# Kernel tuning notes

Measured on AMD Instinct MI355X. Metric: run time of the kernel, lower is better.

The kernel has to match this reference:

```python
import jax, jax.numpy as jnp
import numpy as np

NW = 30000      # num_words (word nodes)
ND = 8192       # num_docs
D = 300         # hidden_dim
D2 = D // 2
NNZ_A = 600000  # nnz of word-word adjacency A_norm [NW, NW]
NNZ_X = 524288  # nnz of doc-word tfidf X [ND, NW]
ALPHA = 0.7     # residual_alpha
LN_EPS = 1e-5
BN_SCALE = float(1.0 / np.sqrt(1.0 + 1e-5))  # eval BN, running_mean=0, running_var=1


def _xavier(k, shape):
    fan_out, fan_in = shape[0], shape[1]
    lim = float(np.sqrt(6.0 / (fan_in + fan_out)))
    return jax.random.uniform(k, shape, jnp.float32, -lim, lim)


def setup_inputs() -> dict:
    key = jax.random.key(0)
    ks = jax.random.split(key, 13)
    return {
        "a_rows": jax.random.randint(ks[0], (NNZ_A,), 0, NW, dtype=jnp.int32),
        "a_cols": jax.random.randint(ks[1], (NNZ_A,), 0, NW, dtype=jnp.int32),
        "a_vals": jax.random.uniform(ks[2], (NNZ_A,), jnp.float32) * 0.05,
        "x_rows": jax.random.randint(ks[3], (NNZ_X,), 0, ND, dtype=jnp.int32),
        "x_cols": jax.random.randint(ks[4], (NNZ_X,), 0, NW, dtype=jnp.int32),
        "x_vals": jax.random.uniform(ks[5], (NNZ_X,), jnp.float32) * 0.05,
        "emb": _xavier(ks[6], (NW, D)),
        "w1": _xavier(ks[7], (D, D)),
        "w2": _xavier(ks[8], (D, D)),
        "w3": _xavier(ks[9], (D, D)),
        "ln_g": jnp.ones((D,), jnp.float32),
        "ln_b": jnp.zeros((D,), jnp.float32),
        "m_w1": _xavier(ks[10], (D, D)),
        "m_b1": jnp.zeros((D,), jnp.float32),
        "bn1_g": jnp.ones((D,), jnp.float32),
        "bn1_b": jnp.zeros((D,), jnp.float32),
        "m_w2": _xavier(ks[11], (D2, D)),
        "m_b2": jnp.zeros((D2,), jnp.float32),
        "bn2_g": jnp.ones((D2,), jnp.float32),
        "bn2_b": jnp.zeros((D2,), jnp.float32),
        "clf_w": _xavier(ks[12], (2, D2)),
        "clf_b": jnp.zeros((2,), jnp.float32),
    }


def _spmm(rows, cols, vals, H, n):
    # sparse [n, m] @ dense [m, d] via gather + segment-sum (COO SpMM)
    return jax.ops.segment_sum(vals[:, None] * H[cols], rows, num_segments=n)


def _layernorm(x, g, b):
    mu = jnp.mean(x, axis=-1, keepdims=True)
    var = jnp.var(x, axis=-1, keepdims=True)
    return (x - mu) * jax.lax.rsqrt(var + LN_EPS) * g + b


def _bn_eval(x, g, b):
    # BatchNorm1d in eval mode with freshly-initialized running stats (mean=0, var=1)
    return x * (g * BN_SCALE) + b


def reference(a_rows, a_cols, a_vals, x_rows, x_cols, x_vals, emb, w1, w2, w3,
              ln_g, ln_b, m_w1, m_b1, bn1_g, bn1_b, m_w2, m_b2, bn2_g, bn2_b,
              clf_w, clf_b):
    H0 = emb
    H = jax.nn.relu(_spmm(a_rows, a_cols, a_vals, H0, NW) @ w1.T)
    H = jax.nn.relu(_spmm(a_rows, a_cols, a_vals, H, NW) @ w2.T)
    H = jax.nn.relu(_spmm(a_rows, a_cols, a_vals, H, NW) @ w3.T)
    H = (1.0 - ALPHA) * H0 + ALPHA * H
    word_H = _layernorm(H, ln_g, ln_b)
    # --- doc aggregation: X_tfidf @ word_H + X_tfidf @ emb ---
    doc_H = (_spmm(x_rows, x_cols, x_vals, word_H, ND)
             + _spmm(x_rows, x_cols, x_vals, emb, ND))
    # --- MLP head (dropout inactive in eval) ---
    h = jax.nn.relu(_bn_eval(doc_H @ m_w1.T + m_b1, bn1_g, bn1_b))
    h = jax.nn.relu(_bn_eval(h @ m_w2.T + m_b2, bn2_g, bn2_b))
    return h @ clf_w.T + clf_b  # [ND, 2]
```

## Files before the change

### kernel.cpp

```cpp
#include <hip/hip_runtime.h>

#define NW 30000
#define ND 8192
#define DIM 300
#define DIM2 150
#define NNZA 600000
#define NNZX 524288
#define PD 320
#define PD_U 160
#define BN_SCALE 0.99999500003749971f

typedef unsigned int uint;
typedef unsigned short ushort;
typedef __attribute__((ext_vector_type(8))) short bf16x8;
typedef __attribute__((ext_vector_type(4))) float f32x4;
typedef __attribute__((ext_vector_type(4))) uint uint4v;

static inline int cdiv(int a, int b){ return (a + b - 1) / b; }

__device__ __forceinline__ float b2f_lo(uint u){ return __builtin_bit_cast(float, u << 16); }
__device__ __forceinline__ float b2f_hi(uint u){ return __builtin_bit_cast(float, u & 0xffff0000u); }
__device__ __forceinline__ ushort f2b(float f){
  uint u = __builtin_bit_cast(uint, f);
  u += 0x7fffu + ((u >> 16) & 1u);
  return (ushort)(u >> 16);
}
__device__ __forceinline__ uint packb(float x, float y){
  return (uint)f2b(x) | ((uint)f2b(y) << 16);
}

__global__ void k_hist(const int* __restrict__ rows, int n, int* __restrict__ cnt){
  int i = blockIdx.x * blockDim.x + threadIdx.x;
  if (i < n) atomicAdd(&cnt[rows[i]], 1);
}

__global__ void k_copy_int(const int* __restrict__ a, int* __restrict__ b, int n){
  int i = blockIdx.x * blockDim.x + threadIdx.x;
  if (i < n) b[i] = a[i];
}

__global__ __launch_bounds__(1024) void k_bsum(const int* __restrict__ cnt, int n, int* __restrict__ bs){
  __shared__ int sd[1024];
  int t = threadIdx.x;
  int i = blockIdx.x * 1024 + t;
  sd[t] = (i < n) ? cnt[i] : 0;
  __syncthreads();
  #pragma unroll
  for (int o = 512; o > 0; o >>= 1){
    if (t < o) sd[t] += sd[t + o];
    __syncthreads();
  }
  if (t == 0) bs[blockIdx.x] = sd[0];
}

__global__ __launch_bounds__(64) void k_scan_small(int* __restrict__ bs, int nb,
                                                   int* __restrict__ rp, int n){
  int t = threadIdx.x;
  int orig = (t < nb) ? bs[t] : 0;
  int v = orig;
  #pragma unroll
  for (int o = 1; o < 64; o <<= 1){
    int x = __shfl_up(v, o);
    if (t >= o) v += x;
  }
  if (t < nb) bs[t] = v - orig;
  if (t == nb - 1) rp[n] = v;
}

__global__ __launch_bounds__(1024) void k_scan_apply(const int* __restrict__ cnt, int n,
        const int* __restrict__ bs, int* __restrict__ rp){
  __shared__ int sd[1024];
  int t = threadIdx.x;
  int i = blockIdx.x * 1024 + t;
  int v = (i < n) ? cnt[i] : 0;
  sd[t] = v;
  __syncthreads();
  for (int o = 1; o < 1024; o <<= 1){
    int x = (t >= o) ? sd[t - o] : 0;
    __syncthreads();
    sd[t] += x;
    __syncthreads();
  }
  if (i < n) rp[i] = bs[blockIdx.x] + sd[t] - v;
}

__global__ void k_scatter(const int* __restrict__ rows, const int* __restrict__ cols,
                          const float* __restrict__ vals, int n, int* __restrict__ cursor,
                          int* __restrict__ cs, float* __restrict__ vs){
  int i = blockIdx.x * blockDim.x + threadIdx.x;
  if (i < n){
    int r = rows[i];
    int p = atomicAdd(&cursor[r], 1);
    cs[p] = cols[i];
    vs[p] = vals[i];
  }
}

__global__ void k_f2b_pad8(const float* __restrict__ src, ushort* __restrict__ dst,
                           int srows, int scols, int drows, int dstride){
  int q = blockIdx.x * blockDim.x + threadIdx.x;
  int perRow = dstride >> 3;
  int r = q / perRow;
  int c = (q - r * perRow) << 3;
  if (r >= drows) return;
  float x[8];
  #pragma unroll
  for (int j = 0; j < 8; ++j)
    x[j] = (r < srows && c + j < scols) ? src[(size_t)r * scols + c + j] : 0.f;
  uint4v o;
  o.x = packb(x[0], x[1]); o.y = packb(x[2], x[3]);
  o.z = packb(x[4], x[5]); o.w = packb(x[6], x[7]);
  *(uint4v*)(dst + (size_t)r * dstride + c) = o;
}

__global__ __launch_bounds__(256) void k_spmm_b(const int* __restrict__ rp, const int* __restrict__ cs,
        const float* __restrict__ vs, const uint* __restrict__ Hb, uint* __restrict__ Ob, int nrows){
  int wid = (blockIdx.x * blockDim.x + threadIdx.x) >> 6;
  int lane = threadIdx.x & 63;
  if (wid >= nrows) return;
  int s = rp[wid], e = rp[wid + 1];
  const bool half = lane < 32;
  float acc[4][6] = {};
  int k = s;
  for (; k + 4 <= e; k += 4){
    #pragma unroll
    for (int j = 0; j < 4; ++j){
      int c = cs[k + j];
      float v = vs[k + j];
      const uint* p = Hb + (size_t)c * PD_U;
      uint u0 = p[lane], u1 = p[lane + 64];
      uint u2 = half ? p[lane + 128] : 0;
      acc[j][0] = fmaf(v, b2f_lo(u0), acc[j][0]);
      acc[j][1] = fmaf(v, b2f_hi(u0), acc[j][1]);
      acc[j][2] = fmaf(v, b2f_lo(u1), acc[j][2]);
      acc[j][3] = fmaf(v, b2f_hi(u1), acc[j][3]);
      acc[j][4] = fmaf(v, b2f_lo(u2), acc[j][4]);
      acc[j][5] = fmaf(v, b2f_hi(u2), acc[j][5]);
    }
  }
  for (; k < e; ++k){
    int c = cs[k];
    float v = vs[k];
    const uint* p = Hb + (size_t)c * PD_U;
    uint u0 = p[lane], u1 = p[lane + 64];
    uint u2 = half ? p[lane + 128] : 0;
    acc[0][0] = fmaf(v, b2f_lo(u0), acc[0][0]);
    acc[0][1] = fmaf(v, b2f_hi(u0), acc[0][1]);
    acc[0][2] = fmaf(v, b2f_lo(u1), acc[0][2]);
    acc[0][3] = fmaf(v, b2f_hi(u1), acc[0][3]);
    acc[0][4] = fmaf(v, b2f_lo(u2), acc[0][4]);
    acc[0][5] = fmaf(v, b2f_hi(u2), acc[0][5]);
  }
  #pragma unroll
  for (int d = 0; d < 6; ++d)
    acc[0][d] += (acc[1][d] + acc[2][d]) + acc[3][d];
  uint* o = Ob + (size_t)wid * PD_U;
  o[lane] = packb(acc[0][0], acc[0][1]);
  o[lane + 64] = packb(acc[0][2], acc[0][3]);
  if (half) o[lane + 128] = packb(acc[0][4], acc[0][5]);
}

__global__ __launch_bounds__(256) void k_mgemm(const ushort* __restrict__ A, const ushort* __restrict__ B,
        const float* __restrict__ bias, const float* __restrict__ bng, const float* __restrict__ bnb,
        ushort* __restrict__ C, int M, int Nvalid, int ldc, int relu){
  __shared__ ushort As[128][72];
  __shared__ ushort Bs[160][72];
  const int t = threadIdx.x;
  const int wid = t >> 6, lane = t & 63;
  const int bm = blockIdx.y << 7;
  const int bn = blockIdx.x * 160;
  const int wm = (wid >> 1) << 6;
  const int wn = (wid & 1) * 80;
  const int r16 = lane & 15;
  const int h8 = (lane >> 4) << 3;
  f32x4 acc[4][5] = {};
  for (int k0 = 0; k0 < PD; k0 += 64){
    #pragma unroll
    for (int i = 0; i < 4; ++i){
      int q = t + (i << 8);
      int r = q >> 3, c = (q & 7) << 3;
      int gm = bm + r; if (gm >= M) gm = M - 1;
      *(bf16x8*)(&As[r][c]) = *(const bf16x8*)(A + (size_t)gm * PD + k0 + c);
    }
    #pragma unroll
    for (int i = 0; i < 5; ++i){
      int q = t + (i << 8);
      int r = q >> 3, c = (q & 7) << 3;
      *(bf16x8*)(&Bs[r][c]) = *(const bf16x8*)(B + (size_t)(bn + r) * PD + k0 + c);
    }
    __syncthreads();
    #pragma unroll
    for (int kk = 0; kk < 2; ++kk){
      bf16x8 af[4], bfr[5];
      #pragma unroll
      for (int m = 0; m < 4; ++m)
        af[m] = *(const bf16x8*)(&As[wm + m * 16 + r16][kk * 32 + h8]);
      #pragma unroll
      for (int n = 0; n < 5; ++n)
        bfr[n] = *(const bf16x8*)(&Bs[wn + n * 16 + r16][kk * 32 + h8]);
      #pragma unroll
      for (int m = 0; m < 4; ++m)
        #pragma unroll
        for (int n = 0; n < 5; ++n)
          acc[m][n] = __builtin_amdgcn_mfma_f32_16x16x32_bf16(af[m], bfr[n], acc[m][n], 0, 0, 0);
    }
    __syncthreads();
  }
  const int cr = (lane >> 4) << 2;
  #pragma unroll
  for (int m = 0; m < 4; ++m){
    #pragma unroll
    for (int n = 0; n < 5; ++n){
      int col = bn + wn + n * 16 + r16;
      #pragma unroll
      for (int j = 0; j < 4; ++j){
        int row = bm + wm + m * 16 + cr + j;
        if (row >= M) continue;
        float v = acc[m][n][j];
        if (col < Nvalid){
          if (bias) v += bias[col];
          if (bng)  v = v * (bng[col] * BN_SCALE) + bnb[col];
          if (relu) v = fmaxf(v, 0.f);
        } else v = 0.f;
        C[(size_t)row * ldc + col] = f2b(v);
      }
    }
  }
}

__global__ __launch_bounds__(64) void k_res_ln(const float* __restrict__ emb, const uint* __restrict__ Hb,
        const float* __restrict__ g, const float* __restrict__ bb, uint* __restrict__ S){
  int row = blockIdx.x, lane = threadIdx.x;
  const float* e = emb + (size_t)row * DIM;
  const uint* h = Hb + (size_t)row * PD_U;
  float x[6], ev[6];
  float sum = 0.f, sq = 0.f;
  #pragma unroll
  for (int j = 0; j < 3; ++j){
    int i = lane + j * 64;
    float e0 = 0.f, e1 = 0.f, h0 = 0.f, h1 = 0.f;
    if (i < 150){
      uint u = h[i];
      h0 = b2f_lo(u); h1 = b2f_hi(u);
      e0 = e[2 * i]; e1 = e[2 * i + 1];
    }
    float v0 = 0.3f * e0 + 0.7f * h0;
    float v1 = 0.3f * e1 + 0.7f * h1;
    if (i >= 150){ v0 = 0.f; v1 = 0.f; }
    x[2*j] = v0; x[2*j+1] = v1; ev[2*j] = e0; ev[2*j+1] = e1;
    sum += v0 + v1; sq += v0 * v0 + v1 * v1;
  }
  #pragma unroll
  for (int o = 32; o > 0; o >>= 1){ sum += __shfl_down(sum, o); sq += __shfl_down(sq, o); }
  sum = __shfl(sum, 0); sq = __shfl(sq, 0);
  const float inv = 1.f / (float)DIM;
  float mu = sum * inv;
  float var = sq * inv - mu * mu;
  float rs = rsqrtf(var + 1e-5f);
  uint* o = S + (size_t)row * PD_U;
  #pragma unroll
  for (int j = 0; j < 3; ++j){
    int i = lane + j * 64;
    if (i >= PD_U) continue;
    uint w = 0;
    if (i < 150){
      float r0 = (x[2*j]   - mu) * rs * g[2*i]   + bb[2*i]   + ev[2*j];
      float r1 = (x[2*j+1] - mu) * rs * g[2*i+1] + bb[2*i+1] + ev[2*j+1];
      w = packb(r0, r1);
    }
    o[i] = w;
  }
}

__global__ void k_clf(const uint* __restrict__ h2, const float* __restrict__ w,
                      const float* __restrict__ bias, float* __restrict__ out){
  int m = blockIdx.x * blockDim.x + threadIdx.x;
  if (m >= ND) return;
  const uint* hr = h2 + (size_t)m * 80;
  float s0 = bias[0], s1 = bias[1];
  #pragma unroll 5
  for (int i = 0; i < 75; ++i){
    uint u = hr[i];
    float h0 = b2f_lo(u), h1 = b2f_hi(u);
    int k = 2 * i;
    s0 = fmaf(h0, w[k], fmaf(h1, w[k + 1], s0));
    s1 = fmaf(h0, w[DIM2 + k], fmaf(h1, w[DIM2 + k + 1], s1));
  }
  out[m * 2] = s0;
  out[m * 2 + 1] = s1;
}

extern "C" void kernel_launch(void* const* d_in, const int* in_sizes, int n_in,
                              void* d_out, int out_size, void* d_ws, size_t ws_size,
                              hipStream_t stream){
  const int*   a_rows = (const int*)  d_in[0];
  const int*   a_cols = (const int*)  d_in[1];
  const float* a_vals = (const float*)d_in[2];
  const int*   x_rows = (const int*)  d_in[3];
  const int*   x_cols = (const int*)  d_in[4];
  const float* x_vals = (const float*)d_in[5];
  const float* emb    = (const float*)d_in[6];
  const float* w1     = (const float*)d_in[7];
  const float* w2     = (const float*)d_in[8];
  const float* w3     = (const float*)d_in[9];
  const float* ln_g   = (const float*)d_in[10];
  const float* ln_b   = (const float*)d_in[11];
  const float* m_w1   = (const float*)d_in[12];
  const float* m_b1   = (const float*)d_in[13];
  const float* bn1_g  = (const float*)d_in[14];
  const float* bn1_b  = (const float*)d_in[15];
  const float* m_w2   = (const float*)d_in[16];
  const float* m_b2   = (const float*)d_in[17];
  const float* bn2_g  = (const float*)d_in[18];
  const float* bn2_b  = (const float*)d_in[19];
  const float* clf_w  = (const float*)d_in[20];
  const float* clf_b  = (const float*)d_in[21];
  float* out = (float*)d_out;

  char* ws = (char*)d_ws;
  size_t off = 0;
  auto take = [&](size_t nbytes)->void*{
    void* p = ws + off;
    off += (nbytes + 255) & ~(size_t)255;
    return p;
  };
  int*    a_rp   = (int*)   take((NW + 1) * 4);
  int*    a_cs   = (int*)   take((size_t)NNZA * 4);
  float*  a_vs   = (float*) take((size_t)NNZA * 4);
  int*    x_rp   = (int*)   take((ND + 1) * 4);
  int*    x_cs   = (int*)   take((size_t)NNZX * 4);
  float*  x_vs   = (float*) take((size_t)NNZX * 4);
  int*    cursor = (int*)   take((size_t)NW * 4);
  int*    bsums  = (int*)   take(64 * 4);
  ushort* embb   = (ushort*)take((size_t)NW * PD * 2);
  ushort* Tb     = (ushort*)take((size_t)NW * PD * 2);
  ushort* Hb     = (ushort*)take((size_t)NW * PD * 2);
  ushort* w1b    = (ushort*)take((size_t)PD * PD * 2);
  ushort* w2b    = (ushort*)take((size_t)PD * PD * 2);
  ushort* w3b    = (ushort*)take((size_t)PD * PD * 2);
  ushort* mw1b   = (ushort*)take((size_t)PD * PD * 2);
  ushort* mw2b   = (ushort*)take((size_t)PD * PD * 2);
  ushort* docHb = Hb;
  ushort* h1b   = Hb + (size_t)ND * PD;
  ushort* h2b   = Hb + (size_t)2 * ND * PD;

  int nbA = cdiv(NW, 1024);
  hipMemsetAsync(cursor, 0, NW * 4, stream);
  k_hist<<<cdiv(NNZA, 256), 256, 0, stream>>>(a_rows, NNZA, cursor);
  k_bsum<<<nbA, 1024, 0, stream>>>(cursor, NW, bsums);
  k_scan_small<<<1, 64, 0, stream>>>(bsums, nbA, a_rp, NW);
  k_scan_apply<<<nbA, 1024, 0, stream>>>(cursor, NW, bsums, a_rp);
  k_copy_int<<<cdiv(NW, 256), 256, 0, stream>>>(a_rp, cursor, NW);
  k_scatter<<<cdiv(NNZA, 256), 256, 0, stream>>>(a_rows, a_cols, a_vals, NNZA, cursor, a_cs, a_vs);
  int nbX = cdiv(ND, 1024);
  hipMemsetAsync(cursor, 0, ND * 4, stream);
  k_hist<<<cdiv(NNZX, 256), 256, 0, stream>>>(x_rows, NNZX, cursor);
  k_bsum<<<nbX, 1024, 0, stream>>>(cursor, ND, bsums);
  k_scan_small<<<1, 64, 0, stream>>>(bsums, nbX, x_rp, ND);
  k_scan_apply<<<nbX, 1024, 0, stream>>>(cursor, ND, bsums, x_rp);
  k_copy_int<<<cdiv(ND, 256), 256, 0, stream>>>(x_rp, cursor, ND);
  k_scatter<<<cdiv(NNZX, 256), 256, 0, stream>>>(x_rows, x_cols, x_vals, NNZX, cursor, x_cs, x_vs);

  k_f2b_pad8<<<cdiv(NW * 40, 256), 256, 0, stream>>>(emb, embb, NW, DIM, NW, PD);
  k_f2b_pad8<<<cdiv(PD * 40, 256), 256, 0, stream>>>(w1, w1b, DIM, DIM, PD, PD);
  k_f2b_pad8<<<cdiv(PD * 40, 256), 256, 0, stream>>>(w2, w2b, DIM, DIM, PD, PD);
  k_f2b_pad8<<<cdiv(PD * 40, 256), 256, 0, stream>>>(w3, w3b, DIM, DIM, PD, PD);
  k_f2b_pad8<<<cdiv(PD * 40, 256), 256, 0, stream>>>(m_w1, mw1b, DIM, DIM, PD, PD);
  k_f2b_pad8<<<cdiv(PD * 40, 256), 256, 0, stream>>>(m_w2, mw2b, DIM2, DIM, PD, PD);

  dim3 gg(2, cdiv(NW, 128));
  k_spmm_b<<<cdiv(NW, 4), 256, 0, stream>>>(a_rp, a_cs, a_vs, (const uint*)embb, (uint*)Tb, NW);
  k_mgemm<<<gg, 256, 0, stream>>>(Tb, w1b, nullptr, nullptr, nullptr, Hb, NW, DIM, PD, 1);
  k_spmm_b<<<cdiv(NW, 4), 256, 0, stream>>>(a_rp, a_cs, a_vs, (const uint*)Hb, (uint*)Tb, NW);
  k_mgemm<<<gg, 256, 0, stream>>>(Tb, w2b, nullptr, nullptr, nullptr, Hb, NW, DIM, PD, 1);
  k_spmm_b<<<cdiv(NW, 4), 256, 0, stream>>>(a_rp, a_cs, a_vs, (const uint*)Hb, (uint*)Tb, NW);
  k_mgemm<<<gg, 256, 0, stream>>>(Tb, w3b, nullptr, nullptr, nullptr, Hb, NW, DIM, PD, 1);
  k_res_ln<<<NW, 64, 0, stream>>>(emb, (const uint*)Hb, ln_g, ln_b, (uint*)Tb);
  k_spmm_b<<<cdiv(ND, 4), 256, 0, stream>>>(x_rp, x_cs, x_vs, (const uint*)Tb, (uint*)docHb, ND);
  dim3 g1(2, cdiv(ND, 128));
  k_mgemm<<<g1, 256, 0, stream>>>(docHb, mw1b, m_b1, bn1_g, bn1_b, h1b, ND, DIM, PD, 1);
  dim3 g2(1, cdiv(ND, 128));
  k_mgemm<<<g2, 256, 0, stream>>>(h1b, mw2b, m_b2, bn2_g, bn2_b, h2b, ND, DIM2, 160, 1);
  k_clf<<<cdiv(ND, 256), 256, 0, stream>>>((const uint*)h2b, clf_w, clf_b, out);
}
```

Measured before the change: 557.9 us.

## Split SpMM feature dimension into column slices with multiple rows per wave

Replaces the one-row-per-wave SpMM with a kernel that cuts the 160-uint padded feature row into 8 slices of 20 uints. Each wave handles 3 rows at 20 lanes per row, so slices are spread across blocks. The aim is to keep each block's gather working set (a column slice of H) small enough to stay in cache, and to stop wasting lanes on the padded third load. In exchange, column indices and values are reloaded once per slice (8x index traffic), rows in a wave are padded to the longest row length, and 4 lanes per wave sit idle.

```diff
diff --git a/kernel.cpp b/kernel.cpp
--- a/kernel.cpp
+++ b/kernel.cpp
@@ -113,51 +113,40 @@
   *(uint4v*)(dst + (size_t)r * dstride + c) = o;
 }
 
-__global__ __launch_bounds__(256) void k_spmm_b(const int* __restrict__ rp, const int* __restrict__ cs,
+__global__ __launch_bounds__(256) void k_spmm_sl(const int* __restrict__ rp, const int* __restrict__ cs,
         const float* __restrict__ vs, const uint* __restrict__ Hb, uint* __restrict__ Ob, int nrows){
-  int wid = (blockIdx.x * blockDim.x + threadIdx.x) >> 6;
-  int lane = threadIdx.x & 63;
-  if (wid >= nrows) return;
-  int s = rp[wid], e = rp[wid + 1];
-  const bool half = lane < 32;
-  float acc[4][6] = {};
-  int k = s;
-  for (; k + 4 <= e; k += 4){
-    #pragma unroll
-    for (int j = 0; j < 4; ++j){
-      int c = cs[k + j];
-      float v = vs[k + j];
-      const uint* p = Hb + (size_t)c * PD_U;
-      uint u0 = p[lane], u1 = p[lane + 64];
-      uint u2 = half ? p[lane + 128] : 0;
-      acc[j][0] = fmaf(v, b2f_lo(u0), acc[j][0]);
-      acc[j][1] = fmaf(v, b2f_hi(u0), acc[j][1]);
-      acc[j][2] = fmaf(v, b2f_lo(u1), acc[j][2]);
-      acc[j][3] = fmaf(v, b2f_hi(u1), acc[j][3]);
-      acc[j][4] = fmaf(v, b2f_lo(u2), acc[j][4]);
-      acc[j][5] = fmaf(v, b2f_hi(u2), acc[j][5]);
-    }
-  }
-  for (; k < e; ++k){
-    int c = cs[k];
-    float v = vs[k];
-    const uint* p = Hb + (size_t)c * PD_U;
-    uint u0 = p[lane], u1 = p[lane + 64];
-    uint u2 = half ? p[lane + 128] : 0;
-    acc[0][0] = fmaf(v, b2f_lo(u0), acc[0][0]);
-    acc[0][1] = fmaf(v, b2f_hi(u0), acc[0][1]);
-    acc[0][2] = fmaf(v, b2f_lo(u1), acc[0][2]);
-    acc[0][3] = fmaf(v, b2f_hi(u1), acc[0][3]);
-    acc[0][4] = fmaf(v, b2f_lo(u2), acc[0][4]);
-    acc[0][5] = fmaf(v, b2f_hi(u2), acc[0][5]);
-  }
-  #pragma unroll
-  for (int d = 0; d < 6; ++d)
-    acc[0][d] += (acc[1][d] + acc[2][d]) + acc[3][d];
-  uint* o = Ob + (size_t)wid * PD_U;
-  o[lane] = packb(acc[0][0], acc[0][1]);
-  o[lane + 64] = packb(acc[0][2], acc[0][3]);
-  if (half) o[lane + 128] = packb(acc[0][4], acc[0][5]);
+  const int b  = blockIdx.x;
+  const int sl = b & 7;
+  const int rb = b >> 3;
+  const int wv = threadIdx.x >> 6;
+  const int lane = threadIdx.x & 63;
+  const int rl = lane / 20;
+  const int c  = lane - rl * 20;
+  const int row = (rb * 4 + wv) * 3 + rl;
+  const bool act = (rl < 3) && (row < nrows);
+  int s = 0, e = 0;
+  if (act){ s = rp[row]; e = rp[row + 1]; }
+  int len = e - s;
+  int mx = len;
+  #pragma unroll
+  for (int o = 32; o > 0; o >>= 1) mx = max(mx, __shfl_down(mx, o));
+  mx = __shfl(mx, 0);
+  const uint* base = Hb + sl * 20 + c;
+  float aL0 = 0.f, aH0 = 0.f, aL1 = 0.f, aH1 = 0.f;
+  for (int i = 0; i < mx; i += 2){
+    int k0 = s + i, k1 = s + i + 1;
+    bool p0 = act && (k0 < e);
+    bool p1 = act && (k1 < e);
+    int  c0 = p0 ? cs[k0] : 0;
+    int  c1 = p1 ? cs[k1] : 0;
+    float v0 = p0 ? vs[k0] : 0.f;
+    float v1 = p1 ? vs[k1] : 0.f;
+    uint u0 = p0 ? base[(size_t)c0 * PD_U] : 0u;
+    uint u1 = p1 ? base[(size_t)c1 * PD_U] : 0u;
+    aL0 = fmaf(v0, b2f_lo(u0), aL0); aH0 = fmaf(v0, b2f_hi(u0), aH0);
+    aL1 = fmaf(v1, b2f_lo(u1), aL1); aH1 = fmaf(v1, b2f_hi(u1), aH1);
+  }
+  if (act) Ob[(size_t)row * PD_U + sl * 20 + c] = packb(aL0 + aL1, aH0 + aH1);
 }
 
 __global__ __launch_bounds__(256) void k_mgemm(const ushort* __restrict__ A, const ushort* __restrict__ B,
@@ -368,15 +357,17 @@
   k_f2b_pad8<<<cdiv(PD * 40, 256), 256, 0, stream>>>(m_w1, mw1b, DIM, DIM, PD, PD);
   k_f2b_pad8<<<cdiv(PD * 40, 256), 256, 0, stream>>>(m_w2, mw2b, DIM2, DIM, PD, PD);
 
+  int gsA = cdiv(NW, 12) * 8;
+  int gsX = cdiv(ND, 12) * 8;
   dim3 gg(2, cdiv(NW, 128));
-  k_spmm_b<<<cdiv(NW, 4), 256, 0, stream>>>(a_rp, a_cs, a_vs, (const uint*)embb, (uint*)Tb, NW);
+  k_spmm_sl<<<gsA, 256, 0, stream>>>(a_rp, a_cs, a_vs, (const uint*)embb, (uint*)Tb, NW);
   k_mgemm<<<gg, 256, 0, stream>>>(Tb, w1b, nullptr, nullptr, nullptr, Hb, NW, DIM, PD, 1);
-  k_spmm_b<<<cdiv(NW, 4), 256, 0, stream>>>(a_rp, a_cs, a_vs, (const uint*)Hb, (uint*)Tb, NW);
+  k_spmm_sl<<<gsA, 256, 0, stream>>>(a_rp, a_cs, a_vs, (const uint*)Hb, (uint*)Tb, NW);
   k_mgemm<<<gg, 256, 0, stream>>>(Tb, w2b, nullptr, nullptr, nullptr, Hb, NW, DIM, PD, 1);
-  k_spmm_b<<<cdiv(NW, 4), 256, 0, stream>>>(a_rp, a_cs, a_vs, (const uint*)Hb, (uint*)Tb, NW);
+  k_spmm_sl<<<gsA, 256, 0, stream>>>(a_rp, a_cs, a_vs, (const uint*)Hb, (uint*)Tb, NW);
   k_mgemm<<<gg, 256, 0, stream>>>(Tb, w3b, nullptr, nullptr, nullptr, Hb, NW, DIM, PD, 1);
   k_res_ln<<<NW, 64, 0, stream>>>(emb, (const uint*)Hb, ln_g, ln_b, (uint*)Tb);
-  k_spmm_b<<<cdiv(ND, 4), 256, 0, stream>>>(x_rp, x_cs, x_vs, (const uint*)Tb, (uint*)docHb, ND);
+  k_spmm_sl<<<gsX, 256, 0, stream>>>(x_rp, x_cs, x_vs, (const uint*)Tb, (uint*)docHb, ND);
   dim3 g1(2, cdiv(ND, 128));
   k_mgemm<<<g1, 256, 0, stream>>>(docHb, mw1b, m_b1, bn1_g, bn1_b, h1b, ND, DIM, PD, 1);
   dim3 g2(1, cdiv(ND, 128));
```

Measured after the change: 920.8 us. 65.1% more time.
